# Kernel optimization log

Hardware: AMD Instinct MI355X
Metric: run time of the kernel (lower is better)

Reference implementation:

```python
import jax, jax.numpy as jnp
import numpy as np

HEADS = 4
OUT_DIM = 64
NEG_SLOPE = 0.2


def setup_inputs() -> dict:
    key = jax.random.key(0)
    k1, k2, k3, k4 = jax.random.split(key, 4)
    n, in_dim = 4096, 256
    x = jax.random.normal(k1, (n, in_dim), dtype=jnp.float32)
    adj = jax.random.randint(k2, (n, n), 0, 2, dtype=jnp.int32)
    # lin: in_dim -> heads*out_dim (no bias), stored as [in_dim, heads*out_dim]
    W = jax.random.normal(k3, (in_dim, HEADS * OUT_DIM), dtype=jnp.float32) * 0.05
    # att_weight: [heads, 2*out_dim]
    att = jax.random.normal(k4, (HEADS, 2 * OUT_DIM), dtype=jnp.float32) * 0.05
    return {"x": x, "adj": adj, "W": W, "att": att}


def reference(x, adj, W, att):
    n = x.shape[0]
    h = (x @ W).reshape(n, HEADS, OUT_DIM)  # [n, H, D]
    # scores[i,j,h] = att[h] . cat(h_i, h_j) = <h_i, a_src[h]> + <h_j, a_dst[h]>
    a_src, a_dst = att[:, :OUT_DIM], att[:, OUT_DIM:]
    e_src = jnp.einsum('nhd,hd->nh', h, a_src)  # [n, H]
    e_dst = jnp.einsum('nhd,hd->nh', h, a_dst)  # [n, H]
    scores = e_src[:, None, :] + e_dst[None, :, :]  # [n, n, H]
    scores = jax.nn.leaky_relu(scores, negative_slope=NEG_SLOPE)
    mask = (adj > 0)[:, :, None]  # [n, n, 1]
    scores = jnp.where(mask, scores, -jnp.inf)
    alpha = jax.nn.softmax(scores, axis=1)  # softmax over neighbors j
    # h_prime[i,h,d] = sum_j alpha[i,j,h] * h[j,h,d]
    h_prime = jnp.einsum('ijh,jhd->ihd', alpha, h)
    return h_prime.reshape(n, HEADS * OUT_DIM)
```

## Files before the change

### kernel.cpp

```cpp
#include <hip/hip_runtime.h>
#include <hip/hip_bf16.h>

#define HEADS 4
#define ODIM 64
#define HD 256
#define NEG_SLOPE 0.2f
#define SPLITS 4
#define BJ 128

typedef __attribute__((ext_vector_type(8))) short bf16x8;
typedef __attribute__((ext_vector_type(4))) float floatx4;
typedef __attribute__((ext_vector_type(2))) float floatx2;

__global__ __launch_bounds__(256) void pack_xw(const float* __restrict__ x,
                                               const float* __restrict__ W,
                                               __hip_bfloat16* __restrict__ xh,
                                               __hip_bfloat16* __restrict__ xl,
                                               __hip_bfloat16* __restrict__ wh,
                                               __hip_bfloat16* __restrict__ wl,
                                               int K, int nxb) {
    const int b = blockIdx.x;
    const int Kc = K >> 5;
    if (b < nxb) {
        const int g = b * 256 + threadIdx.x;
        const int lane = g & 63, frag = g >> 6;
        const int kc = frag % Kc, mc = frag / Kc;
        const int l16 = lane & 15, q = lane >> 4;
        const float* src = x + (size_t)(mc * 16 + l16) * K + kc * 32 + q * 8;
        const float4 v0 = *(const float4*)src;
        const float4 v1 = *(const float4*)(src + 4);
        const float vv[8] = {v0.x, v0.y, v0.z, v0.w, v1.x, v1.y, v1.z, v1.w};
        union { __hip_bfloat16 b[8]; bf16x8 v; } H, L;
        #pragma unroll
        for (int p = 0; p < 8; ++p) {
            H.b[p] = __float2bfloat16(vv[p]);
            L.b[p] = __float2bfloat16(vv[p] - __bfloat162float(H.b[p]));
        }
        *(bf16x8*)&xh[(size_t)frag * 512 + lane * 8] = H.v;
        *(bf16x8*)&xl[(size_t)frag * 512 + lane * 8] = L.v;
    } else {
        const int g = (b - nxb) * 256 + threadIdx.x;
        const int lane = g & 63, frag = g >> 6;
        const int kc = frag % Kc, nc = frag / Kc;
        const int l16 = lane & 15, q = lane >> 4;
        union { __hip_bfloat16 b[8]; bf16x8 v; } H, L;
        #pragma unroll
        for (int p = 0; p < 8; ++p) {
            const float w = W[(size_t)(kc * 32 + q * 8 + p) * HD + nc * 16 + l16];
            H.b[p] = __float2bfloat16(w);
            L.b[p] = __float2bfloat16(w - __bfloat162float(H.b[p]));
        }
        *(bf16x8*)&wh[(size_t)frag * 512 + lane * 8] = H.v;
        *(bf16x8*)&wl[(size_t)frag * 512 + lane * 8] = L.v;
    }
}

__global__ __launch_bounds__(128) void gemm_fused(
    const __hip_bfloat16* __restrict__ xh, const __hip_bfloat16* __restrict__ xl,
    const __hip_bfloat16* __restrict__ wh, const __hip_bfloat16* __restrict__ wl,
    const float* __restrict__ att, float4* __restrict__ E4,
    __hip_bfloat16* __restrict__ hbB, int n, int K) {

    __shared__ __hip_bfloat16 T[64][40];

    const int tid = threadIdx.x, wave = tid >> 6, lane = tid & 63;
    const int q = lane >> 4, l16 = lane & 15;
    const int m0 = blockIdx.x * 32;
    const int head = blockIdx.y;
    const int Kc = K >> 5;
    const int mc = (m0 >> 4) + wave;

    floatx4 acc[4] = {{0.f,0.f,0.f,0.f},{0.f,0.f,0.f,0.f},{0.f,0.f,0.f,0.f},{0.f,0.f,0.f,0.f}};

    const __hip_bfloat16* Axh = xh + (size_t)mc * Kc * 512 + lane * 8;
    const __hip_bfloat16* Axl = xl + (size_t)mc * Kc * 512 + lane * 8;
    const __hip_bfloat16* Bwh = wh + lane * 8;
    const __hip_bfloat16* Bwl = wl + lane * 8;
    #pragma unroll 2
    for (int kc = 0; kc < Kc; ++kc) {
        const bf16x8 ah = *(const bf16x8*)(Axh + (size_t)kc * 512);
        const bf16x8 al = *(const bf16x8*)(Axl + (size_t)kc * 512);
        bf16x8 bh[4], bl[4];
        #pragma unroll
        for (int nt = 0; nt < 4; ++nt) {
            const size_t fo = (size_t)((head * 4 + nt) * Kc + kc) * 512;
            bh[nt] = *(const bf16x8*)(Bwh + fo);
            bl[nt] = *(const bf16x8*)(Bwl + fo);
        }
        #pragma unroll
        for (int nt = 0; nt < 4; ++nt)
            acc[nt] = __builtin_amdgcn_mfma_f32_16x16x32_bf16(ah, bh[nt], acc[nt], 0, 0, 0);
        #pragma unroll
        for (int nt = 0; nt < 4; ++nt)
            acc[nt] = __builtin_amdgcn_mfma_f32_16x16x32_bf16(ah, bl[nt], acc[nt], 0, 0, 0);
        #pragma unroll
        for (int nt = 0; nt < 4; ++nt)
            acc[nt] = __builtin_amdgcn_mfma_f32_16x16x32_bf16(al, bh[nt], acc[nt], 0, 0, 0);
    }

    float as_v[4], ad_v[4];
    #pragma unroll
    for (int nt = 0; nt < 4; ++nt) {
        as_v[nt] = att[head * 2 * ODIM + nt * 16 + l16];
        ad_v[nt] = att[head * 2 * ODIM + ODIM + nt * 16 + l16];
    }
    #pragma unroll
    for (int r = 0; r < 4; ++r) {
        float ps = 0.f, pd = 0.f;
        #pragma unroll
        for (int nt = 0; nt < 4; ++nt) {
            ps = fmaf(acc[nt][r], as_v[nt], ps);
            pd = fmaf(acc[nt][r], ad_v[nt], pd);
        }
        #pragma unroll
        for (int m = 1; m <= 8; m <<= 1) {
            ps += __shfl_xor(ps, m, 64);
            pd += __shfl_xor(pd, m, 64);
        }
        if (l16 == 0) {
            const int i = m0 + wave * 16 + q * 4 + r;
            E4[i * HEADS + head] = make_float4(__expf(ps), __expf(NEG_SLOPE * ps),
                                               __expf(pd), __expf(NEG_SLOPE * pd));
        }
    }

    #pragma unroll
    for (int nt = 0; nt < 4; ++nt) {
        union { __hip_bfloat16 b[4]; uint2 u; } pk;
        #pragma unroll
        for (int r = 0; r < 4; ++r) pk.b[r] = __float2bfloat16(acc[nt][r]);
        *(uint2*)&T[nt * 16 + l16][wave * 16 + q * 4] = pk.u;
    }
    __syncthreads();

    #pragma unroll
    for (int ffi = 0; ffi < 2; ++ffi) {
        const int f = wave + ffi * 2;
        const bf16x8 v = *(const bf16x8*)&T[f * 16 + l16][q * 8];
        const size_t frag = ((size_t)head * (n >> 5) + (m0 >> 5)) * 4 + f;
        *(bf16x8*)&hbB[frag * 512 + lane * 8] = v;
    }
}

__global__ __launch_bounds__(256, 2) void aggregate(
    const int* __restrict__ adj, const float4* __restrict__ E4,
    const __hip_bfloat16* __restrict__ hbB, float* __restrict__ outsp,
    float* __restrict__ densp, int n, int KR) {

    __shared__ unsigned short adjL[2][32][136];
    __shared__ float2 EdL[2][HEADS][BJ];

    const int tid = threadIdx.x;
    const int wave = tid >> 6, lane = tid & 63;
    const int q = lane >> 4, l16 = lane & 15, q8 = (lane >> 4) * 8;
    const int i0 = blockIdx.x * 32;
    const int K0 = blockIdx.y * KR;

    const int sr = tid >> 3, sg = (tid & 7) * 16;
    const int je = tid >> 1, heb = (tid & 1) * 2;

    floatx2 es12[2];
    #pragma unroll
    for (int mt = 0; mt < 2; ++mt) {
        const float4 e = E4[(i0 + mt * 16 + l16) * HEADS + wave];
        es12[mt][0] = e.x; es12[mt][1] = e.y;
    }

    union { short s[8]; bf16x8 v; } bones;
    #pragma unroll
    for (int p = 0; p < 8; ++p) bones.s[p] = (l16 == 0) ? (short)0x3F80 : (short)0;

    floatx4 acc[2][4];
    floatx4 accd[2];
    #pragma unroll
    for (int mt = 0; mt < 2; ++mt) {
        accd[mt] = (floatx4){0.f, 0.f, 0.f, 0.f};
        #pragma unroll
        for (int nt = 0; nt < 4; ++nt) acc[mt][nt] = (floatx4){0.f, 0.f, 0.f, 0.f};
    }

    const int* aprow = &adj[(size_t)(i0 + sr) * n];
    const size_t fragbase = (size_t)wave * (n >> 5) * 4;

    int4 ajA[4], ajB[4];
    float4 evA0, evA1, evB0, evB1;

    auto loadPref = [&](int jc, int4* aj, float4& e0, float4& e1) {
        const int4* ap = (const int4*)(aprow + jc + sg);
        aj[0] = ap[0]; aj[1] = ap[1]; aj[2] = ap[2]; aj[3] = ap[3];
        e0 = E4[(jc + je) * HEADS + heb];
        e1 = E4[(jc + je) * HEADS + heb + 1];
    };
    auto stage = [&](int buf, const int4* aj, const float4& e0, const float4& e1) {
        const int* av = (const int*)aj;
        #pragma unroll
        for (int g2 = 0; g2 < 2; ++g2) {
            uint4 u;
            u.x = (av[g2*8+0] > 0 ? 0xFFFFu : 0u) | (av[g2*8+1] > 0 ? 0xFFFF0000u : 0u);
            u.y = (av[g2*8+2] > 0 ? 0xFFFFu : 0u) | (av[g2*8+3] > 0 ? 0xFFFF0000u : 0u);
            u.z = (av[g2*8+4] > 0 ? 0xFFFFu : 0u) | (av[g2*8+5] > 0 ? 0xFFFF0000u : 0u);
            u.w = (av[g2*8+6] > 0 ? 0xFFFFu : 0u) | (av[g2*8+7] > 0 ? 0xFFFF0000u : 0u);
            *(uint4*)&adjL[buf][sr][sg + g2 * 8] = u;
        }
        EdL[buf][heb][je]     = make_float2(e0.z, e0.w);
        EdL[buf][heb + 1][je] = make_float2(e1.z, e1.w);
    };

    auto computeChunk = [&](int buf, int jc) {
        bf16x8 bA[4], bB[4];
        #pragma unroll
        for (int nt = 0; nt < 4; ++nt)
            bA[nt] = *(const bf16x8*)&hbB[(fragbase + (size_t)(jc >> 5) * 4 + nt) * 512 + lane * 8];
        #pragma unroll
        for (int ks = 0; ks < 4; ++ks) {
            const bf16x8* bcur = (ks & 1) ? bB : bA;
            bf16x8* bnxt = (ks & 1) ? bA : bB;
            if (ks < 3) {
                #pragma unroll
                for (int nt = 0; nt < 4; ++nt)
                    bnxt[nt] = *(const bf16x8*)&hbB[(fragbase + (size_t)((jc >> 5) + ks + 1) * 4 + nt) * 512 + lane * 8];
            }
            const float4* ep = (const float4*)&EdL[buf][wave][ks * 32 + q8];
            const float4 e01 = ep[0], e23 = ep[1], e45 = ep[2], e67 = ep[3];
            floatx2 ed[8];
            ed[0][0]=e01.x; ed[0][1]=e01.y;  ed[1][0]=e01.z; ed[1][1]=e01.w;
            ed[2][0]=e23.x; ed[2][1]=e23.y;  ed[3][0]=e23.z; ed[3][1]=e23.w;
            ed[4][0]=e45.x; ed[4][1]=e45.y;  ed[5][0]=e45.z; ed[5][1]=e45.w;
            ed[6][0]=e67.x; ed[6][1]=e67.y;  ed[7][0]=e67.z; ed[7][1]=e67.w;
            #pragma unroll
            for (int mt = 0; mt < 2; ++mt) {
                const uint4 msk = *(const uint4*)&adjL[buf][mt * 16 + l16][ks * 32 + q8];
                const unsigned int mm[4] = {msk.x, msk.y, msk.z, msk.w};
                union { unsigned int u[4]; bf16x8 v; } af;
                #pragma unroll
                for (int p = 0; p < 4; ++p) {
                    const floatx2 pa = es12[mt] * ed[2 * p];
                    const floatx2 pb = es12[mt] * ed[2 * p + 1];
                    const float wa = fmaxf(pa[0], pa[1]);
                    const float wb = fmaxf(pb[0], pb[1]);
                    af.u[p] = __builtin_amdgcn_perm(__float_as_uint(wb), __float_as_uint(wa),
                                                    0x07060302u) & mm[p];
                }
                #pragma unroll
                for (int nt = 0; nt < 4; ++nt)
                    acc[mt][nt] = __builtin_amdgcn_mfma_f32_16x16x32_bf16(af.v, bcur[nt], acc[mt][nt], 0, 0, 0);
                accd[mt] = __builtin_amdgcn_mfma_f32_16x16x32_bf16(af.v, bones.v, accd[mt], 0, 0, 0);
            }
        }
    };

    const int KEND = K0 + KR;
    loadPref(K0, ajA, evA0, evA1);
    loadPref(K0 + BJ < KEND ? K0 + BJ : K0, ajB, evB0, evB1);
    stage(0, ajA, evA0, evA1);
    __syncthreads();

    for (int jc = K0; jc < KEND; jc += 2 * BJ) {
        int j2 = jc + 2 * BJ; if (j2 >= KEND) j2 = K0;
        loadPref(j2, ajA, evA0, evA1);
        computeChunk(0, jc);
        stage(1, ajB, evB0, evB1);
        __syncthreads();

        int j3 = jc + 3 * BJ; if (j3 >= KEND) j3 = K0;
        loadPref(j3, ajB, evB0, evB1);
        computeChunk(1, jc + BJ);
        stage(0, ajA, evA0, evA1);
        __syncthreads();
    }

    const size_t sOut = (size_t)blockIdx.y * n * HD;
    #pragma unroll
    for (int mt = 0; mt < 2; ++mt)
        #pragma unroll
        for (int nt = 0; nt < 4; ++nt)
            #pragma unroll
            for (int r = 0; r < 4; ++r)
                outsp[sOut + (size_t)(i0 + mt * 16 + q * 4 + r) * HD + wave * ODIM + nt * 16 + l16] = acc[mt][nt][r];
    if (l16 == 0) {
        #pragma unroll
        for (int mt = 0; mt < 2; ++mt)
            #pragma unroll
            for (int r = 0; r < 4; ++r)
                densp[((size_t)blockIdx.y * n + i0 + mt * 16 + q * 4 + r) * HEADS + wave] = accd[mt][r];
    }
}

__global__ __launch_bounds__(256) void normalize(const float* __restrict__ outsp,
                                                 const float* __restrict__ densp,
                                                 float* __restrict__ out, int n, int splits) {
    const int g = blockIdx.x * 256 + threadIdx.x;
    const int i = g >> 6;
    const int c4 = (g & 63) * 4;
    const int head = c4 >> 6;
    float den = 0.f;
    for (int s = 0; s < splits; ++s) den += densp[((size_t)s * n + i) * HEADS + head];
    float4 v = {0.f, 0.f, 0.f, 0.f};
    for (int s = 0; s < splits; ++s) {
        const float4 t = *(const float4*)&outsp[(size_t)s * n * HD + (size_t)i * HD + c4];
        v.x += t.x; v.y += t.y; v.z += t.z; v.w += t.w;
    }
    const float inv = 1.0f / den;
    v.x *= inv; v.y *= inv; v.z *= inv; v.w *= inv;
    *(float4*)&out[(size_t)i * HD + c4] = v;
}

extern "C" void kernel_launch(void* const* d_in, const int* in_sizes, int n_in,
                              void* d_out, int out_size, void* d_ws, size_t ws_size,
                              hipStream_t stream) {
    const float* x   = (const float*)d_in[0];
    const int*   adj = (const int*)d_in[1];
    const float* W   = (const float*)d_in[2];
    const float* att = (const float*)d_in[3];
    float* out = (float*)d_out;

    const int in_dim = in_sizes[2] / HD;
    const int n = in_sizes[0] / in_dim;

    char* ws = (char*)d_ws;
    size_t off = 0;
    auto alloc = [&](size_t bytes) -> void* {
        void* p = ws + off; off += (bytes + 255) & ~(size_t)255; return p;
    };
    __hip_bfloat16* xh = (__hip_bfloat16*)alloc((size_t)n * in_dim * 2);
    __hip_bfloat16* xl = (__hip_bfloat16*)alloc((size_t)n * in_dim * 2);
    __hip_bfloat16* wh = (__hip_bfloat16*)alloc((size_t)in_dim * HD * 2);
    __hip_bfloat16* wl = (__hip_bfloat16*)alloc((size_t)in_dim * HD * 2);
    float4*         E4 = (float4*)alloc((size_t)n * HEADS * 16);
    __hip_bfloat16* hbB = (__hip_bfloat16*)alloc((size_t)n * HD * 2);

    const size_t outB = (size_t)n * HD * 4, denB = (size_t)n * HEADS * 4;
    float* densp = (float*)alloc((size_t)SPLITS * denB);
    float* outsp = (float*)alloc((size_t)SPLITS * outB);

    const int nxb = (n / 16) * (in_dim / 32) * 64 / 256;
    const int nwb = (HD / 16) * (in_dim / 32) * 64 / 256;
    pack_xw<<<nxb + nwb, 256, 0, stream>>>(x, W, xh, xl, wh, wl, in_dim, nxb);
    gemm_fused<<<dim3(n / 32, HEADS), 128, 0, stream>>>(xh, xl, wh, wl, att, E4, hbB, n, in_dim);
    aggregate<<<dim3(n / 32, SPLITS), 256, 0, stream>>>(adj, E4, hbB, outsp, densp, n, n / SPLITS);
    normalize<<<n * 64 / 256, 256, 0, stream>>>(outsp, densp, out, n, SPLITS);
}
```

Baseline: 143.6 us.

## Compress adjacency to bitmask and drop LDS staging in aggregate

Adds a pre-pass kernel that uses wave ballots to turn the int32 adjacency matrix into a packed bitmask. The aggregate kernel then reads mask words and per-head destination scores straight from global memory with register double-buffering, replacing the LDS staging, barriers and repeated int32 adjacency reads. Per-node scores are split into head-major src/dst float2 arrays for contiguous loads. The full 64 MB adjacency is still read once by the new kernel, and every wave now fetches mask and score data from global memory itself.

```diff
diff --git a/kernel.cpp b/kernel.cpp
--- a/kernel.cpp
+++ b/kernel.cpp
@@ -6,7 +6,6 @@
 #define HD 256
 #define NEG_SLOPE 0.2f
 #define SPLITS 4
-#define BJ 128
 
 typedef __attribute__((ext_vector_type(8))) short bf16x8;
 typedef __attribute__((ext_vector_type(4))) float floatx4;
@@ -55,10 +54,31 @@
     }
 }
 
+__global__ __launch_bounds__(256) void compress_adj(const int* __restrict__ adj,
+                                                    unsigned int* __restrict__ bits, int n) {
+    const int wid = (blockIdx.x * 256 + threadIdx.x) >> 6;
+    const int lane = threadIdx.x & 63;
+    const int nq = n >> 10;
+    const int i = wid / nq;
+    const int jb = (wid % nq) << 10;
+    const int nw = n >> 5;
+    #pragma unroll 4
+    for (int jj = 0; jj < 16; ++jj) {
+        const int j = jb + jj * 64 + lane;
+        const unsigned long long m = __ballot(adj[(size_t)i * n + j] > 0);
+        if (lane == 0) {
+            uint2 u;
+            u.x = (unsigned int)m;
+            u.y = (unsigned int)(m >> 32);
+            *(uint2*)&bits[(size_t)i * nw + ((jb + jj * 64) >> 5)] = u;
+        }
+    }
+}
+
 __global__ __launch_bounds__(128) void gemm_fused(
     const __hip_bfloat16* __restrict__ xh, const __hip_bfloat16* __restrict__ xl,
     const __hip_bfloat16* __restrict__ wh, const __hip_bfloat16* __restrict__ wl,
-    const float* __restrict__ att, float4* __restrict__ E4,
+    const float* __restrict__ att, float2* __restrict__ esrc, float2* __restrict__ edst,
     __hip_bfloat16* __restrict__ hbB, int n, int K) {
 
     __shared__ __hip_bfloat16 T[64][40];
@@ -119,8 +139,8 @@
         }
         if (l16 == 0) {
             const int i = m0 + wave * 16 + q * 4 + r;
-            E4[i * HEADS + head] = make_float4(__expf(ps), __expf(NEG_SLOPE * ps),
-                                               __expf(pd), __expf(NEG_SLOPE * pd));
+            esrc[head * n + i] = make_float2(__expf(ps), __expf(NEG_SLOPE * ps));
+            edst[head * n + i] = make_float2(__expf(pd), __expf(NEG_SLOPE * pd));
         }
     }
 
@@ -143,26 +163,21 @@
 }
 
 __global__ __launch_bounds__(256, 2) void aggregate(
-    const int* __restrict__ adj, const float4* __restrict__ E4,
-    const __hip_bfloat16* __restrict__ hbB, float* __restrict__ outsp,
-    float* __restrict__ densp, int n, int KR) {
-
-    __shared__ unsigned short adjL[2][32][136];
-    __shared__ float2 EdL[2][HEADS][BJ];
+    const unsigned int* __restrict__ bits, const float2* __restrict__ esrc,
+    const float2* __restrict__ edst, const __hip_bfloat16* __restrict__ hbB,
+    float* __restrict__ outsp, float* __restrict__ densp, int n, int KR) {
 
     const int tid = threadIdx.x;
     const int wave = tid >> 6, lane = tid & 63;
-    const int q = lane >> 4, l16 = lane & 15, q8 = (lane >> 4) * 8;
+    const int q = lane >> 4, l16 = lane & 15;
     const int i0 = blockIdx.x * 32;
     const int K0 = blockIdx.y * KR;
-
-    const int sr = tid >> 3, sg = (tid & 7) * 16;
-    const int je = tid >> 1, heb = (tid & 1) * 2;
+    const int nw = n >> 5;
 
     floatx2 es12[2];
     #pragma unroll
     for (int mt = 0; mt < 2; ++mt) {
-        const float4 e = E4[(i0 + mt * 16 + l16) * HEADS + wave];
+        const float2 e = esrc[wave * n + i0 + mt * 16 + l16];
         es12[mt][0] = e.x; es12[mt][1] = e.y;
     }
 
@@ -179,94 +194,64 @@
         for (int nt = 0; nt < 4; ++nt) acc[mt][nt] = (floatx4){0.f, 0.f, 0.f, 0.f};
     }
 
-    const int* aprow = &adj[(size_t)(i0 + sr) * n];
-    const size_t fragbase = (size_t)wave * (n >> 5) * 4;
-
-    int4 ajA[4], ajB[4];
-    float4 evA0, evA1, evB0, evB1;
-
-    auto loadPref = [&](int jc, int4* aj, float4& e0, float4& e1) {
-        const int4* ap = (const int4*)(aprow + jc + sg);
-        aj[0] = ap[0]; aj[1] = ap[1]; aj[2] = ap[2]; aj[3] = ap[3];
-        e0 = E4[(jc + je) * HEADS + heb];
-        e1 = E4[(jc + je) * HEADS + heb + 1];
-    };
-    auto stage = [&](int buf, const int4* aj, const float4& e0, const float4& e1) {
-        const int* av = (const int*)aj;
-        #pragma unroll
-        for (int g2 = 0; g2 < 2; ++g2) {
-            uint4 u;
-            u.x = (av[g2*8+0] > 0 ? 0xFFFFu : 0u) | (av[g2*8+1] > 0 ? 0xFFFF0000u : 0u);
-            u.y = (av[g2*8+2] > 0 ? 0xFFFFu : 0u) | (av[g2*8+3] > 0 ? 0xFFFF0000u : 0u);
-            u.z = (av[g2*8+4] > 0 ? 0xFFFFu : 0u) | (av[g2*8+5] > 0 ? 0xFFFF0000u : 0u);
-            u.w = (av[g2*8+6] > 0 ? 0xFFFFu : 0u) | (av[g2*8+7] > 0 ? 0xFFFF0000u : 0u);
-            *(uint4*)&adjL[buf][sr][sg + g2 * 8] = u;
-        }
-        EdL[buf][heb][je]     = make_float2(e0.z, e0.w);
-        EdL[buf][heb + 1][je] = make_float2(e1.z, e1.w);
-    };
-
-    auto computeChunk = [&](int buf, int jc) {
-        bf16x8 bA[4], bB[4];
-        #pragma unroll
-        for (int nt = 0; nt < 4; ++nt)
-            bA[nt] = *(const bf16x8*)&hbB[(fragbase + (size_t)(jc >> 5) * 4 + nt) * 512 + lane * 8];
-        #pragma unroll
-        for (int ks = 0; ks < 4; ++ks) {
-            const bf16x8* bcur = (ks & 1) ? bB : bA;
-            bf16x8* bnxt = (ks & 1) ? bA : bB;
-            if (ks < 3) {
-                #pragma unroll
-                for (int nt = 0; nt < 4; ++nt)
-                    bnxt[nt] = *(const bf16x8*)&hbB[(fragbase + (size_t)((jc >> 5) + ks + 1) * 4 + nt) * 512 + lane * 8];
+    const unsigned int* brow0 = bits + (size_t)(i0 + l16) * nw + (K0 >> 5);
+    const unsigned int* brow1 = bits + (size_t)(i0 + 16 + l16) * nw + (K0 >> 5);
+    const float2* edp = edst + (size_t)wave * n + K0 + q * 8;
+    const __hip_bfloat16* hb = hbB + ((size_t)wave * (n >> 5) + (K0 >> 5)) * 4 * 512 + lane * 8;
+
+    const int NSTEP = KR >> 5;
+
+    unsigned int cw0, cw1; float4 ced[4]; bf16x8 cbf[4];
+    cw0 = brow0[0]; cw1 = brow1[0];
+    {
+        const float4* ep = (const float4*)edp;
+        ced[0] = ep[0]; ced[1] = ep[1]; ced[2] = ep[2]; ced[3] = ep[3];
+        #pragma unroll
+        for (int nt = 0; nt < 4; ++nt)
+            cbf[nt] = *(const bf16x8*)&hb[(size_t)nt * 512];
+    }
+
+    for (int s = 0; s < NSTEP; ++s) {
+        unsigned int nw0, nw1; float4 ned[4]; bf16x8 nbf[4];
+        const int sn = (s + 1 < NSTEP) ? s + 1 : s;
+        nw0 = brow0[sn]; nw1 = brow1[sn];
+        {
+            const float4* ep = (const float4*)(edp + (size_t)sn * 32);
+            ned[0] = ep[0]; ned[1] = ep[1]; ned[2] = ep[2]; ned[3] = ep[3];
+            #pragma unroll
+            for (int nt = 0; nt < 4; ++nt)
+                nbf[nt] = *(const bf16x8*)&hb[((size_t)sn * 4 + nt) * 512];
+        }
+
+        #pragma unroll
+        for (int mt = 0; mt < 2; ++mt) {
+            const unsigned int bm = ((mt ? cw1 : cw0) >> (q * 8)) & 0xFFu;
+            union { unsigned int u[4]; bf16x8 v; } af;
+            #pragma unroll
+            for (int p = 0; p < 4; ++p) {
+                const float4 e = ced[p];
+                floatx2 e0; e0[0] = e.x; e0[1] = e.y;
+                floatx2 e1; e1[0] = e.z; e1[1] = e.w;
+                const floatx2 pa = es12[mt] * e0;
+                const floatx2 pb = es12[mt] * e1;
+                const float wa = fmaxf(pa[0], pa[1]);
+                const float wb = fmaxf(pb[0], pb[1]);
+                const unsigned int b2 = (bm >> (2 * p)) & 3u;
+                const unsigned int mm = (b2 & 1u) * 0xFFFFu | (b2 >> 1) * 0xFFFF0000u;
+                af.u[p] = __builtin_amdgcn_perm(__float_as_uint(wb), __float_as_uint(wa),
+                                                0x07060302u) & mm;
             }
-            const float4* ep = (const float4*)&EdL[buf][wave][ks * 32 + q8];
-            const float4 e01 = ep[0], e23 = ep[1], e45 = ep[2], e67 = ep[3];
-            floatx2 ed[8];
-            ed[0][0]=e01.x; ed[0][1]=e01.y;  ed[1][0]=e01.z; ed[1][1]=e01.w;
-            ed[2][0]=e23.x; ed[2][1]=e23.y;  ed[3][0]=e23.z; ed[3][1]=e23.w;
-            ed[4][0]=e45.x; ed[4][1]=e45.y;  ed[5][0]=e45.z; ed[5][1]=e45.w;
-            ed[6][0]=e67.x; ed[6][1]=e67.y;  ed[7][0]=e67.z; ed[7][1]=e67.w;
-            #pragma unroll
-            for (int mt = 0; mt < 2; ++mt) {
-                const uint4 msk = *(const uint4*)&adjL[buf][mt * 16 + l16][ks * 32 + q8];
-                const unsigned int mm[4] = {msk.x, msk.y, msk.z, msk.w};
-                union { unsigned int u[4]; bf16x8 v; } af;
-                #pragma unroll
-                for (int p = 0; p < 4; ++p) {
-                    const floatx2 pa = es12[mt] * ed[2 * p];
-                    const floatx2 pb = es12[mt] * ed[2 * p + 1];
-                    const float wa = fmaxf(pa[0], pa[1]);
-                    const float wb = fmaxf(pb[0], pb[1]);
-                    af.u[p] = __builtin_amdgcn_perm(__float_as_uint(wb), __float_as_uint(wa),
-                                                    0x07060302u) & mm[p];
-                }
-                #pragma unroll
-                for (int nt = 0; nt < 4; ++nt)
-                    acc[mt][nt] = __builtin_amdgcn_mfma_f32_16x16x32_bf16(af.v, bcur[nt], acc[mt][nt], 0, 0, 0);
-                accd[mt] = __builtin_amdgcn_mfma_f32_16x16x32_bf16(af.v, bones.v, accd[mt], 0, 0, 0);
-            }
-        }
-    };
-
-    const int KEND = K0 + KR;
-    loadPref(K0, ajA, evA0, evA1);
-    loadPref(K0 + BJ < KEND ? K0 + BJ : K0, ajB, evB0, evB1);
-    stage(0, ajA, evA0, evA1);
-    __syncthreads();
-
-    for (int jc = K0; jc < KEND; jc += 2 * BJ) {
-        int j2 = jc + 2 * BJ; if (j2 >= KEND) j2 = K0;
-        loadPref(j2, ajA, evA0, evA1);
-        computeChunk(0, jc);
-        stage(1, ajB, evB0, evB1);
-        __syncthreads();
-
-        int j3 = jc + 3 * BJ; if (j3 >= KEND) j3 = K0;
-        loadPref(j3, ajB, evB0, evB1);
-        computeChunk(1, jc + BJ);
-        stage(0, ajA, evA0, evA1);
-        __syncthreads();
+            #pragma unroll
+            for (int nt = 0; nt < 4; ++nt)
+                acc[mt][nt] = __builtin_amdgcn_mfma_f32_16x16x32_bf16(af.v, cbf[nt], acc[mt][nt], 0, 0, 0);
+            accd[mt] = __builtin_amdgcn_mfma_f32_16x16x32_bf16(af.v, bones.v, accd[mt], 0, 0, 0);
+        }
+
+        cw0 = nw0; cw1 = nw1;
+        #pragma unroll
+        for (int p = 0; p < 4; ++p) ced[p] = ned[p];
+        #pragma unroll
+        for (int nt = 0; nt < 4; ++nt) cbf[nt] = nbf[nt];
     }
 
     const size_t sOut = (size_t)blockIdx.y * n * HD;
@@ -326,8 +311,10 @@
     __hip_bfloat16* xl = (__hip_bfloat16*)alloc((size_t)n * in_dim * 2);
     __hip_bfloat16* wh = (__hip_bfloat16*)alloc((size_t)in_dim * HD * 2);
     __hip_bfloat16* wl = (__hip_bfloat16*)alloc((size_t)in_dim * HD * 2);
-    float4*         E4 = (float4*)alloc((size_t)n * HEADS * 16);
+    float2* esrc = (float2*)alloc((size_t)HEADS * n * 8);
+    float2* edst = (float2*)alloc((size_t)HEADS * n * 8);
     __hip_bfloat16* hbB = (__hip_bfloat16*)alloc((size_t)n * HD * 2);
+    unsigned int* bits = (unsigned int*)alloc((size_t)n * (n / 8));
 
     const size_t outB = (size_t)n * HD * 4, denB = (size_t)n * HEADS * 4;
     float* densp = (float*)alloc((size_t)SPLITS * denB);
@@ -336,7 +323,8 @@
     const int nxb = (n / 16) * (in_dim / 32) * 64 / 256;
     const int nwb = (HD / 16) * (in_dim / 32) * 64 / 256;
     pack_xw<<<nxb + nwb, 256, 0, stream>>>(x, W, xh, xl, wh, wl, in_dim, nxb);
-    gemm_fused<<<dim3(n / 32, HEADS), 128, 0, stream>>>(xh, xl, wh, wl, att, E4, hbB, n, in_dim);
-    aggregate<<<dim3(n / 32, SPLITS), 256, 0, stream>>>(adj, E4, hbB, outsp, densp, n, n / SPLITS);
+    compress_adj<<<(n * (n >> 10)) / 4, 256, 0, stream>>>(adj, bits, n);
+    gemm_fused<<<dim3(n / 32, HEADS), 128, 0, stream>>>(xh, xl, wh, wl, att, esrc, edst, hbB, n, in_dim);
+    aggregate<<<dim3(n / 32, SPLITS), 256, 0, stream>>>(bits, esrc, edst, hbB, outsp, densp, n, n / SPLITS);
     normalize<<<n * 64 / 256, 256, 0, stream>>>(outsp, densp, out, n, SPLITS);
 }
```

After: 166.9 us. 16.2% more time.
